# Optimization experiments

Measured on AMD Instinct MI355X. Metric: run time of the kernel, lower is better.

## Reference

```python
import jax, jax.numpy as jnp
import numpy as np

N_TOKENS = 8192
D_MODEL = 1024
N_EXPERT = 8
TOP_K = 2
D_HIDDEN = 4 * D_MODEL


def setup_inputs() -> dict:
    key = jax.random.key(0)
    ks = jax.random.split(key, 7)
    s_in = 1.0 / np.sqrt(D_MODEL)
    s_hid = 1.0 / np.sqrt(D_HIDDEN)
    return {
        "inp": jax.random.normal(ks[0], (N_TOKENS, D_MODEL), dtype=jnp.float32),
        "gate_w": jax.random.normal(ks[1], (D_MODEL, N_EXPERT), dtype=jnp.float32) * s_in,
        "gate_b": jnp.zeros((N_EXPERT,), dtype=jnp.float32),
        "w1": jax.random.normal(ks[2], (N_EXPERT, D_MODEL, D_HIDDEN), dtype=jnp.float32) * s_in,
        "b1": jnp.zeros((N_EXPERT, D_HIDDEN), dtype=jnp.float32),
        "w2": jax.random.normal(ks[3], (N_EXPERT, D_HIDDEN, D_MODEL), dtype=jnp.float32) * s_hid,
        "b2": jnp.zeros((N_EXPERT, D_MODEL), dtype=jnp.float32),
    }


def reference(inp, gate_w, gate_b, w1, b1, w2, b2):
    # NaiveGate: linear logits -> top_k -> softmax over the selected k logits
    logits = inp @ gate_w + gate_b                      # [N, E]
    top_vals, top_idx = jax.lax.top_k(logits, TOP_K)    # [N, K]
    gate_score = jax.nn.softmax(top_vals, axis=-1)      # [N, K]

    # Dispatch/combine: y[n] = sum_k score[n,k] * expert_{idx[n,k]}(x[n]).
    # Loop over the small fixed expert set; mask-weighted accumulate replaces
    # the scatter / grouped-GEMM / gather of the original (same math).
    y = jnp.zeros_like(inp)
    for e in range(N_EXPERT):
        h = jax.nn.gelu(inp @ w1[e] + b1[e])             # [N, H]
        o = h @ w2[e] + b2[e]                            # [N, D]
        w_e = jnp.sum(gate_score * (top_idx == e), axis=-1)  # [N]
        y = y + w_e[:, None] * o
    return y
```

## Files before the change

kernel.cpp:

```cpp
#include <hip/hip_runtime.h>
#include <hip/hip_bf16.h>

#define NT 8192
#define DM 1024
#define NE 8
#define DH 4096
#define NP (NT * 2)

typedef __attribute__((ext_vector_type(8))) __bf16 bf16x8;
typedef __attribute__((ext_vector_type(4))) float f32x4;

__device__ __forceinline__ ushort f2bf(float f) {
  unsigned int x = __float_as_uint(f);
  unsigned int r = (x + 0x7fffu + ((x >> 16) & 1u)) >> 16;
  return (ushort)r;
}

__device__ __forceinline__ float gelu_fast(float x) {
  float x2 = x * x;
  float t = __builtin_fmaf(x2, 0.044715f, 1.0f);
  float m = x * t * 2.3025851f;
  m = fminf(m, 126.0f);
  float p = __builtin_amdgcn_exp2f(m);
  return x * p * __builtin_amdgcn_rcpf(p + 1.0f);
}

__device__ __forceinline__ void async_copy16(const void* gsrc, void* ldst) {
  __builtin_amdgcn_global_load_lds(
      (const __attribute__((address_space(1))) void*)gsrc,
      (__attribute__((address_space(3))) void*)ldst, 16, 0, 0);
}

__global__ __launch_bounds__(256) void fused_pre_kernel(
    const float* __restrict__ w1, const float* __restrict__ w2,
    ushort* __restrict__ w1t, ushort* __restrict__ w2t,
    const float* __restrict__ inp, const float* __restrict__ gw,
    const float* __restrict__ gb, ushort* __restrict__ inp_bf,
    int* __restrict__ counts, int* __restrict__ tok_list,
    float* __restrict__ scale_list, float* __restrict__ y) {
  __shared__ ushort tileT[128][136];
  __shared__ int   lcnt[NE];
  __shared__ int   gbase[NE];
  __shared__ int   ltok[NE][64];
  __shared__ float lsc[NE][64];
  const int b = blockIdx.x;

  if (b < 128) {
    const int t = threadIdx.x;
    if (t < NE) lcnt[t] = 0;
    __syncthreads();
    const int wave = t >> 6, lane = t & 63;
    const int tokBase = b * 64 + wave * 16;
    for (int ti = 0; ti < 16; ti++) {
      const int token = tokBase + ti;
      const float* x = inp + (size_t)token * DM;
      float acc[NE];
#pragma unroll
      for (int e = 0; e < NE; e++) acc[e] = 0.f;
#pragma unroll
      for (int j = 0; j < 16; j++) {
        int idx = j * 64 + lane;
        float xv = x[idx];
        const float4* g = (const float4*)(gw + (size_t)idx * NE);
        float4 g0 = g[0], g1 = g[1];
        acc[0] += xv * g0.x; acc[1] += xv * g0.y; acc[2] += xv * g0.z; acc[3] += xv * g0.w;
        acc[4] += xv * g1.x; acc[5] += xv * g1.y; acc[6] += xv * g1.z; acc[7] += xv * g1.w;
      }
#pragma unroll
      for (int e = 0; e < NE; e++) {
        for (int off = 32; off; off >>= 1) acc[e] += __shfl_xor(acc[e], off, 64);
      }
      if (lane == 0) {
        float v[NE];
#pragma unroll
        for (int e = 0; e < NE; e++) v[e] = acc[e] + gb[e];
        int i0 = 0; float b0 = v[0];
#pragma unroll
        for (int e = 1; e < NE; e++) if (v[e] > b0) { b0 = v[e]; i0 = e; }
        int i1 = -1; float b1v = -INFINITY;
#pragma unroll
        for (int e = 0; e < NE; e++) if (e != i0 && v[e] > b1v) { b1v = v[e]; i1 = e; }
        float s1 = 1.f / (1.f + __expf(b0 - b1v));
        float s0 = 1.f - s1;
        int p0 = atomicAdd(&lcnt[i0], 1);
        ltok[i0][p0] = token; lsc[i0][p0] = s0;
        int p1 = atomicAdd(&lcnt[i1], 1);
        ltok[i1][p1] = token; lsc[i1][p1] = s1;
      }
    }
    __syncthreads();
    if (t < NE) gbase[t] = atomicAdd(&counts[t], lcnt[t]);
    __syncthreads();
#pragma unroll
    for (int e = 0; e < NE; e++) {
      int n = lcnt[e], gb0 = gbase[e];
      for (int s = t; s < n; s += 256) {
        tok_list[e * NT + gb0 + s] = ltok[e][s];
        scale_list[e * NT + gb0 + s] = lsc[e][s];
      }
    }
  } else if (b < 4224) {
    const int tb = b - 128;
    const int which = tb >> 11;
    const int rem = tb & 2047;
    const int e = rem >> 8;
    const int bb = rem & 255;
    const float* src;
    ushort* dst;
    int R, C, r0, c0;
    if (which == 0) {
      src = w1 + (size_t)e * DM * DH; dst = w1t + (size_t)e * DM * DH;
      R = DM; C = DH;
      r0 = (bb & 7) * 128;   c0 = (bb >> 3) * 128;
    } else {
      src = w2 + (size_t)e * DM * DH; dst = w2t + (size_t)e * DM * DH;
      R = DH; C = DM;
      r0 = (bb & 31) * 128;  c0 = (bb >> 5) * 128;
    }
    const int tx = threadIdx.x & 31;
    const int ty = threadIdx.x >> 5;
#pragma unroll
    for (int i = 0; i < 4; i++) {
      int rb = ty + 8 * i;
      const float* sp = src + (size_t)(r0 + 4 * rb) * C + c0 + 4 * tx;
      float4 a0 = *(const float4*)(sp);
      float4 a1 = *(const float4*)(sp + C);
      float4 a2 = *(const float4*)(sp + 2 * (size_t)C);
      float4 a3 = *(const float4*)(sp + 3 * (size_t)C);
      ushort4 o0 = { f2bf(a0.x), f2bf(a1.x), f2bf(a2.x), f2bf(a3.x) };
      ushort4 o1 = { f2bf(a0.y), f2bf(a1.y), f2bf(a2.y), f2bf(a3.y) };
      ushort4 o2 = { f2bf(a0.z), f2bf(a1.z), f2bf(a2.z), f2bf(a3.z) };
      ushort4 o3 = { f2bf(a0.w), f2bf(a1.w), f2bf(a2.w), f2bf(a3.w) };
      *(ushort4*)(&tileT[4 * tx + 0][4 * rb]) = o0;
      *(ushort4*)(&tileT[4 * tx + 1][4 * rb]) = o1;
      *(ushort4*)(&tileT[4 * tx + 2][4 * rb]) = o2;
      *(ushort4*)(&tileT[4 * tx + 3][4 * rb]) = o3;
    }
    __syncthreads();
    const int kx = threadIdx.x & 31;
    const int ny = threadIdx.x >> 5;
#pragma unroll
    for (int i = 0; i < 16; i++) {
      int n = ny + 8 * i;
      *(ushort4*)(dst + (size_t)(c0 + n) * R + r0 + 4 * kx) =
          *(const ushort4*)(&tileT[n][4 * kx]);
    }
  } else if (b < 6272) {
    const int idx = b - 4224;
    const float4* s4 = (const float4*)(inp + (size_t)idx * 4096);
    ushort4* d4 = (ushort4*)(inp_bf + (size_t)idx * 4096);
    const int t = threadIdx.x;
#pragma unroll
    for (int j = 0; j < 4; j++) {
      float4 v = s4[t + j * 256];
      ushort4 o = { f2bf(v.x), f2bf(v.y), f2bf(v.z), f2bf(v.w) };
      d4[t + j * 256] = o;
    }
  } else {
    const int idx = b - 6272;
    float4* dst = (float4*)(y + (size_t)idx * 4096);
    f32x4 z = {0.f, 0.f, 0.f, 0.f};
#pragma unroll
    for (int j = 0; j < 4; j++)
      ((f32x4*)dst)[j * 256 + threadIdx.x] = z;
  }
}


#define STAGE_TILE(base)                                      \
  do {                                                        \
    async_copy16(aP0, (char*)(base) + wv * 1024);             \
    async_copy16(aP1, (char*)(base) + 4096 + wv * 1024);      \
    async_copy16(bP0, (char*)(base) + 8192 + wv * 1024);      \
    async_copy16(bP1, (char*)(base) + 12288 + wv * 1024);     \
    aP0 += 32; aP1 += 32; bP0 += 32; bP1 += 32;               \
  } while (0)

__global__ __launch_bounds__(256) void gemm1_kernel(
    const ushort* __restrict__ xbf, const ushort* __restrict__ w1t,
    const float* __restrict__ b1, const int* __restrict__ tok_list,
    const int* __restrict__ counts, ushort* __restrict__ hbuf) {
  const int b = blockIdx.x;
  const int e = b & 7;
  const int idx = b >> 3;
  const int mTile = idx & 63;
  const int nTile = idx >> 6;
  int off = 0;
  for (int i = 0; i < e; i++) off += counts[i];
  const int cnt = counts[e];
  if (mTile * 128 >= cnt) return;

  __shared__ __attribute__((aligned(128))) char ldsB[49152];

  const int t = threadIdx.x;
  const int lane = t & 63, wv = t >> 6;
  const int wm = wv & 1, wn = wv >> 1;

  const int sr = t >> 2;
  const int sc = (((t & 3) ^ ((sr >> 1) & 3)) * 8);
  int gi0 = mTile * 128 + sr;      if (gi0 >= cnt) gi0 = cnt - 1;
  int gi1 = mTile * 128 + 64 + sr; if (gi1 >= cnt) gi1 = cnt - 1;
  const int tok0 = tok_list[e * NT + gi0];
  const int tok1 = tok_list[e * NT + gi1];
  const ushort* aP0 = xbf + (size_t)tok0 * DM + sc;
  const ushort* aP1 = xbf + (size_t)tok1 * DM + sc;
  const ushort* bP0 = w1t + ((size_t)e * DH + nTile * 128 + sr) * DM + sc;
  const ushort* bP1 = bP0 + (size_t)64 * DM;

  f32x4 zero = {0.f, 0.f, 0.f, 0.f};
  f32x4 acc[4][4];
#pragma unroll
  for (int i = 0; i < 4; i++)
#pragma unroll
    for (int j = 0; j < 4; j++) acc[i][j] = zero;

  const int quad = lane >> 4, lc = lane & 15;
  const int rq = quad ^ ((lc >> 1) & 3);

  auto compute = [&](const char* buf) {
    const char* A_ = buf;
    const char* B_ = buf + 8192;
    bf16x8 af[4], bfr[4];
#pragma unroll
    for (int mi = 0; mi < 4; mi++) {
      int row = wm * 64 + mi * 16 + lc;
      af[mi] = *(const bf16x8*)(A_ + row * 64 + rq * 16);
    }
#pragma unroll
    for (int ni = 0; ni < 4; ni++) {
      int row = wn * 64 + ni * 16 + lc;
      bfr[ni] = *(const bf16x8*)(B_ + row * 64 + rq * 16);
    }
#pragma unroll
    for (int mi = 0; mi < 4; mi++)
#pragma unroll
      for (int ni = 0; ni < 4; ni++)
        acc[mi][ni] = __builtin_amdgcn_mfma_f32_16x16x32_bf16(af[mi], bfr[ni], acc[mi][ni], 0, 0, 0);
  };

  const int NIT = DM / 32;
  STAGE_TILE(ldsB);
  STAGE_TILE(ldsB + 16384);
  int cur = 0;
  for (int tt = 0; tt < NIT - 1; ++tt) {
    asm volatile("s_waitcnt vmcnt(4)" ::: "memory");
    __builtin_amdgcn_s_barrier();
    if (tt + 2 < NIT) {
      int nx = cur + 2; if (nx >= 3) nx -= 3;
      STAGE_TILE(ldsB + nx * 16384);
    }
    compute(ldsB + cur * 16384);
    cur = (cur == 2) ? 0 : cur + 1;
  }
  asm volatile("s_waitcnt vmcnt(0)" ::: "memory");
  __builtin_amdgcn_s_barrier();
  compute(ldsB + cur * 16384);

  float bias[4];
#pragma unroll
  for (int ni = 0; ni < 4; ni++)
    bias[ni] = b1[(size_t)e * DH + nTile * 128 + wn * 64 + ni * 16 + lc];

#pragma unroll
  for (int mi = 0; mi < 4; mi++) {
#pragma unroll
    for (int r = 0; r < 4; r++) {
      int lr = wm * 64 + mi * 16 + quad * 4 + r;
      int gi = mTile * 128 + lr;
      if (gi < cnt) {
        ushort* hrow = hbuf + (size_t)(off + gi) * DH + nTile * 128 + wn * 64 + lc;
#pragma unroll
        for (int ni = 0; ni < 4; ni++) {
          float v = acc[mi][ni][r] + bias[ni];
          hrow[ni * 16] = f2bf(gelu_fast(v));
        }
      }
    }
  }
}

__global__ __launch_bounds__(256) void gemm2_kernel(
    const ushort* __restrict__ hbuf, const ushort* __restrict__ w2t,
    const float* __restrict__ b2, const int* __restrict__ tok_list,
    const float* __restrict__ scale_list, const int* __restrict__ counts,
    float* __restrict__ y) {
  const int b = blockIdx.x;
  const int e = b & 7;
  const int idx = b >> 3;
  const int nTile = idx & 7;
  const int mTile = idx >> 3;
  int off = 0;
  for (int i = 0; i < e; i++) off += counts[i];
  const int cnt = counts[e];
  if (mTile * 128 >= cnt) return;

  __shared__ __attribute__((aligned(128))) char ldsB[49152];

  const int t = threadIdx.x;
  const int lane = t & 63, wv = t >> 6;
  const int wm = wv & 1, wn = wv >> 1;

  const int sr = t >> 2;
  const int sc = (((t & 3) ^ ((sr >> 1) & 3)) * 8);
  int gi0 = mTile * 128 + sr;      if (gi0 >= cnt) gi0 = cnt - 1;
  int gi1 = mTile * 128 + 64 + sr; if (gi1 >= cnt) gi1 = cnt - 1;
  const ushort* aP0 = hbuf + (size_t)(off + gi0) * DH + sc;
  const ushort* aP1 = hbuf + (size_t)(off + gi1) * DH + sc;
  const ushort* bP0 = w2t + ((size_t)e * DM + nTile * 128 + sr) * DH + sc;
  const ushort* bP1 = bP0 + (size_t)64 * DH;

  f32x4 zero = {0.f, 0.f, 0.f, 0.f};
  f32x4 acc[4][4];
#pragma unroll
  for (int i = 0; i < 4; i++)
#pragma unroll
    for (int j = 0; j < 4; j++) acc[i][j] = zero;

  const int quad = lane >> 4, lc = lane & 15;
  const int rq = quad ^ ((lc >> 1) & 3);

  auto compute = [&](const char* buf) {
    const char* A_ = buf;
    const char* B_ = buf + 8192;
    bf16x8 af[4], bfr[4];
#pragma unroll
    for (int mi = 0; mi < 4; mi++) {
      int row = wm * 64 + mi * 16 + lc;
      af[mi] = *(const bf16x8*)(A_ + row * 64 + rq * 16);
    }
#pragma unroll
    for (int ni = 0; ni < 4; ni++) {
      int row = wn * 64 + ni * 16 + lc;
      bfr[ni] = *(const bf16x8*)(B_ + row * 64 + rq * 16);
    }
#pragma unroll
    for (int mi = 0; mi < 4; mi++)
#pragma unroll
      for (int ni = 0; ni < 4; ni++)
        acc[mi][ni] = __builtin_amdgcn_mfma_f32_16x16x32_bf16(af[mi], bfr[ni], acc[mi][ni], 0, 0, 0);
  };

  const int NIT = DH / 32;
  STAGE_TILE(ldsB);
  STAGE_TILE(ldsB + 16384);
  int cur = 0;
  for (int tt = 0; tt < NIT - 1; ++tt) {
    asm volatile("s_waitcnt vmcnt(4)" ::: "memory");
    __builtin_amdgcn_s_barrier();
    if (tt + 2 < NIT) {
      int nx = cur + 2; if (nx >= 3) nx -= 3;
      STAGE_TILE(ldsB + nx * 16384);
    }
    compute(ldsB + cur * 16384);
    cur = (cur == 2) ? 0 : cur + 1;
  }
  asm volatile("s_waitcnt vmcnt(0)" ::: "memory");
  __builtin_amdgcn_s_barrier();
  compute(ldsB + cur * 16384);

  float bias[4];
#pragma unroll
  for (int ni = 0; ni < 4; ni++)
    bias[ni] = b2[(size_t)e * DM + nTile * 128 + wn * 64 + ni * 16 + lc];

#pragma unroll
  for (int mi = 0; mi < 4; mi++) {
#pragma unroll
    for (int r = 0; r < 4; r++) {
      int lr = wm * 64 + mi * 16 + quad * 4 + r;
      int gi = mTile * 128 + lr;
      if (gi < cnt) {
        int tok = tok_list[e * NT + gi];
        float s = scale_list[e * NT + gi];
        float* yrow = y + (size_t)tok * DM + nTile * 128 + wn * 64 + lc;
#pragma unroll
        for (int ni = 0; ni < 4; ni++) {
          float v = (acc[mi][ni][r] + bias[ni]) * s;
          unsafeAtomicAdd(&yrow[ni * 16], v);
        }
      }
    }
  }
}

extern "C" void kernel_launch(void* const* d_in, const int* in_sizes, int n_in,
                              void* d_out, int out_size, void* d_ws, size_t ws_size,
                              hipStream_t stream) {
  const float* inp = (const float*)d_in[0];
  const float* gw  = (const float*)d_in[1];
  const float* gb  = (const float*)d_in[2];
  const float* w1  = (const float*)d_in[3];
  const float* b1  = (const float*)d_in[4];
  const float* w2  = (const float*)d_in[5];
  const float* b2  = (const float*)d_in[6];
  float* y = (float*)d_out;

  char* ws = (char*)d_ws;
  ushort* inp_bf = (ushort*)ws;              ws += (size_t)NT * DM * 2;
  ushort* w1t    = (ushort*)ws;              ws += (size_t)NE * DH * DM * 2;
  ushort* w2t    = (ushort*)ws;              ws += (size_t)NE * DM * DH * 2;
  ushort* hbuf   = (ushort*)ws;              ws += (size_t)NP * DH * 2;
  int*    tok_list   = (int*)ws;             ws += (size_t)NE * NT * 4;
  float*  scale_list = (float*)ws;           ws += (size_t)NE * NT * 4;
  int*    counts     = (int*)ws;             ws += 256;

  hipMemsetAsync(counts, 0, 256, stream);

  fused_pre_kernel<<<8320, 256, 0, stream>>>(w1, w2, w1t, w2t, inp, gw, gb,
                                             inp_bf, counts, tok_list, scale_list, y);
  gemm1_kernel<<<NE * 32 * 64, 256, 0, stream>>>(inp_bf, w1t, b1, tok_list, counts, hbuf);
  gemm2_kernel<<<NE * 8 * 64, 256, 0, stream>>>(hbuf, w2t, b2, tok_list, scale_list, counts, y);
}
```

Baseline: 752.8 us.

## Rewrite gemm2 with 256x256 tiles, 8 waves and a phased double-buffered pipeline

The down-projection GEMM moves from 128x128 tiles with 4 waves and a 3-stage K=32 ring buffer to 256x256 tiles with 8 waves, K=64 steps and a 128KB double-buffered LDS. Each K step is split into four quadrant phases. Each phase interleaves async global-to-LDS staging of the next tile with MFMA work and raises wave priority around the MFMA bursts. The aim is more operand reuse per byte loaded and better overlap of loads with matrix math. The cost is one block per CU, larger per-tile padding waste for uneven expert counts, and prefetch reads past the end of each row on the final iteration.

```diff
diff --git a/kernel.cpp b/kernel.cpp
--- a/kernel.cpp
+++ b/kernel.cpp
@@ -166,7 +166,6 @@
   }
 }
 
-
 #define STAGE_TILE(base)                                      \
   do {                                                        \
     async_copy16(aP0, (char*)(base) + wv * 1024);             \
@@ -279,7 +278,7 @@
   }
 }
 
-__global__ __launch_bounds__(256) void gemm2_kernel(
+__global__ __launch_bounds__(512, 2) void gemm2_kernel(
     const ushort* __restrict__ hbuf, const ushort* __restrict__ w2t,
     const float* __restrict__ b2, const int* __restrict__ tok_list,
     const float* __restrict__ scale_list, const int* __restrict__ counts,
@@ -287,96 +286,185 @@
   const int b = blockIdx.x;
   const int e = b & 7;
   const int idx = b >> 3;
-  const int nTile = idx & 7;
-  const int mTile = idx >> 3;
+  const int nTile = idx & 3;
+  const int mTile = idx >> 2;
   int off = 0;
   for (int i = 0; i < e; i++) off += counts[i];
   const int cnt = counts[e];
-  if (mTile * 128 >= cnt) return;
-
-  __shared__ __attribute__((aligned(128))) char ldsB[49152];
-
-  const int t = threadIdx.x;
-  const int lane = t & 63, wv = t >> 6;
-  const int wm = wv & 1, wn = wv >> 1;
-
-  const int sr = t >> 2;
-  const int sc = (((t & 3) ^ ((sr >> 1) & 3)) * 8);
-  int gi0 = mTile * 128 + sr;      if (gi0 >= cnt) gi0 = cnt - 1;
-  int gi1 = mTile * 128 + 64 + sr; if (gi1 >= cnt) gi1 = cnt - 1;
-  const ushort* aP0 = hbuf + (size_t)(off + gi0) * DH + sc;
-  const ushort* aP1 = hbuf + (size_t)(off + gi1) * DH + sc;
-  const ushort* bP0 = w2t + ((size_t)e * DM + nTile * 128 + sr) * DH + sc;
-  const ushort* bP1 = bP0 + (size_t)64 * DH;
+  if (mTile * 256 >= cnt) return;
+
+  __shared__ __attribute__((aligned(128))) char ldsB[131072];
+
+  const int tid = threadIdx.x;
+  const int lane = tid & 63;
+  const int wv = tid >> 6;
+  const int wm = wv >> 2;
+  const int wn = wv & 3;
+  const int quad = lane >> 4, lc = lane & 15;
+
+  const int rl0 = tid >> 3;
+  const int rl1 = rl0 + 64;
+  const int s8 = tid & 7;
+  const int k0sw0 = (s8 ^ (rl0 & 7)) * 8;
+  const int k0sw1 = (s8 ^ (rl1 & 7)) * 8;
+  int gA[4];
+#pragma unroll
+  for (int h = 0; h < 2; h++) {
+    int g0 = mTile * 256 + h * 128 + rl0; if (g0 >= cnt) g0 = cnt - 1;
+    int g1 = mTile * 256 + h * 128 + rl1; if (g1 >= cnt) g1 = cnt - 1;
+    gA[h * 2 + 0] = g0; gA[h * 2 + 1] = g1;
+  }
+  const ushort* aP00 = hbuf + (size_t)(off + gA[0]) * DH + k0sw0;
+  const ushort* aP01 = hbuf + (size_t)(off + gA[1]) * DH + k0sw1;
+  const ushort* aP10 = hbuf + (size_t)(off + gA[2]) * DH + k0sw0;
+  const ushort* aP11 = hbuf + (size_t)(off + gA[3]) * DH + k0sw1;
+  const size_t bRow = (size_t)e * DM + nTile * 256;
+  const ushort* bP00 = w2t + (bRow + rl0) * DH + k0sw0;
+  const ushort* bP01 = w2t + (bRow + rl1) * DH + k0sw1;
+  const ushort* bP10 = w2t + (bRow + 128 + rl0) * DH + k0sw0;
+  const ushort* bP11 = w2t + (bRow + 128 + rl1) * DH + k0sw1;
+
+  const int sw0 = ((0 + quad) ^ (lc & 7)) * 16;
+  const int sw1 = ((4 + quad) ^ (lc & 7)) * 16;
+  const int aRow0 = (wm * 64 + lc) * 128;
+  const int bRow0 = (wn * 32 + lc) * 128;
 
   f32x4 zero = {0.f, 0.f, 0.f, 0.f};
-  f32x4 acc[4][4];
-#pragma unroll
-  for (int i = 0; i < 4; i++)
+  f32x4 acc[8][4];
+#pragma unroll
+  for (int i = 0; i < 8; i++)
 #pragma unroll
     for (int j = 0; j < 4; j++) acc[i][j] = zero;
 
-  const int quad = lane >> 4, lc = lane & 15;
-  const int rq = quad ^ ((lc >> 1) & 3);
-
-  auto compute = [&](const char* buf) {
-    const char* A_ = buf;
-    const char* B_ = buf + 8192;
-    bf16x8 af[4], bfr[4];
+  bf16x8 af0[4][2], af1[4][2], bfr[2][2];
+
+#define STG_A0(nbB) do { async_copy16(aP00, (nbB) + tid * 16);                 \
+                         async_copy16(aP01, (nbB) + 8192 + tid * 16); } while (0)
+#define STG_A1(nbB) do { async_copy16(aP10, (nbB) + 16384 + tid * 16);         \
+                         async_copy16(aP11, (nbB) + 16384 + 8192 + tid * 16); } while (0)
+#define STG_B0(nbB) do { async_copy16(bP00, (nbB) + 32768 + tid * 16);         \
+                         async_copy16(bP01, (nbB) + 32768 + 8192 + tid * 16); } while (0)
+#define STG_B1(nbB) do { async_copy16(bP10, (nbB) + 49152 + tid * 16);         \
+                         async_copy16(bP11, (nbB) + 49152 + 8192 + tid * 16); } while (0)
+#define ADV8() do { aP00 += 64; aP01 += 64; aP10 += 64; aP11 += 64;            \
+                    bP00 += 64; bP01 += 64; bP10 += 64; bP11 += 64; } while (0)
+
+  STG_A0(ldsB); STG_B0(ldsB); STG_A1(ldsB); STG_B1(ldsB);
+  ADV8();
+  asm volatile("s_waitcnt vmcnt(4)" ::: "memory");
+  __builtin_amdgcn_s_barrier();
+
+  const int NTIT = DH / 64;
+  for (int t = 0; t < NTIT; ++t) {
+    const char* cA = ldsB + (t & 1) * 65536;
+    const char* cB = cA + 32768;
+    char* nbB = ldsB + ((t & 1) ^ 1) * 65536;
+
 #pragma unroll
     for (int mi = 0; mi < 4; mi++) {
-      int row = wm * 64 + mi * 16 + lc;
-      af[mi] = *(const bf16x8*)(A_ + row * 64 + rq * 16);
-    }
-#pragma unroll
-    for (int ni = 0; ni < 4; ni++) {
-      int row = wn * 64 + ni * 16 + lc;
-      bfr[ni] = *(const bf16x8*)(B_ + row * 64 + rq * 16);
-    }
+      af0[mi][0] = *(const bf16x8*)(cA + aRow0 + mi * 2048 + sw0);
+      af0[mi][1] = *(const bf16x8*)(cA + aRow0 + mi * 2048 + sw1);
+    }
+#pragma unroll
+    for (int j = 0; j < 2; j++) {
+      bfr[j][0] = *(const bf16x8*)(cB + bRow0 + j * 2048 + sw0);
+      bfr[j][1] = *(const bf16x8*)(cB + bRow0 + j * 2048 + sw1);
+    }
+    STG_A0(nbB);
+    asm volatile("s_waitcnt vmcnt(4)" ::: "memory");
+    __builtin_amdgcn_s_barrier();
+    asm volatile("s_waitcnt lgkmcnt(0)" ::: "memory");
+    __builtin_amdgcn_sched_barrier(0);
+    __builtin_amdgcn_s_setprio(1);
 #pragma unroll
     for (int mi = 0; mi < 4; mi++)
 #pragma unroll
-      for (int ni = 0; ni < 4; ni++)
-        acc[mi][ni] = __builtin_amdgcn_mfma_f32_16x16x32_bf16(af[mi], bfr[ni], acc[mi][ni], 0, 0, 0);
-  };
-
-  const int NIT = DH / 32;
-  STAGE_TILE(ldsB);
-  STAGE_TILE(ldsB + 16384);
-  int cur = 0;
-  for (int tt = 0; tt < NIT - 1; ++tt) {
+      for (int j = 0; j < 2; j++) {
+        acc[mi][j] = __builtin_amdgcn_mfma_f32_16x16x32_bf16(af0[mi][0], bfr[j][0], acc[mi][j], 0, 0, 0);
+        acc[mi][j] = __builtin_amdgcn_mfma_f32_16x16x32_bf16(af0[mi][1], bfr[j][1], acc[mi][j], 0, 0, 0);
+      }
+    __builtin_amdgcn_s_setprio(0);
+    __builtin_amdgcn_s_barrier();
+
+#pragma unroll
+    for (int mi = 0; mi < 4; mi++) {
+      af1[mi][0] = *(const bf16x8*)(cA + 16384 + aRow0 + mi * 2048 + sw0);
+      af1[mi][1] = *(const bf16x8*)(cA + 16384 + aRow0 + mi * 2048 + sw1);
+    }
+    STG_B0(nbB);
     asm volatile("s_waitcnt vmcnt(4)" ::: "memory");
     __builtin_amdgcn_s_barrier();
-    if (tt + 2 < NIT) {
-      int nx = cur + 2; if (nx >= 3) nx -= 3;
-      STAGE_TILE(ldsB + nx * 16384);
-    }
-    compute(ldsB + cur * 16384);
-    cur = (cur == 2) ? 0 : cur + 1;
-  }
-  asm volatile("s_waitcnt vmcnt(0)" ::: "memory");
-  __builtin_amdgcn_s_barrier();
-  compute(ldsB + cur * 16384);
+    asm volatile("s_waitcnt lgkmcnt(0)" ::: "memory");
+    __builtin_amdgcn_sched_barrier(0);
+    __builtin_amdgcn_s_setprio(1);
+#pragma unroll
+    for (int mi = 0; mi < 4; mi++)
+#pragma unroll
+      for (int j = 0; j < 2; j++) {
+        acc[4 + mi][j] = __builtin_amdgcn_mfma_f32_16x16x32_bf16(af1[mi][0], bfr[j][0], acc[4 + mi][j], 0, 0, 0);
+        acc[4 + mi][j] = __builtin_amdgcn_mfma_f32_16x16x32_bf16(af1[mi][1], bfr[j][1], acc[4 + mi][j], 0, 0, 0);
+      }
+    __builtin_amdgcn_s_setprio(0);
+    __builtin_amdgcn_s_barrier();
+
+#pragma unroll
+    for (int j = 0; j < 2; j++) {
+      bfr[j][0] = *(const bf16x8*)(cB + 16384 + bRow0 + j * 2048 + sw0);
+      bfr[j][1] = *(const bf16x8*)(cB + 16384 + bRow0 + j * 2048 + sw1);
+    }
+    STG_A1(nbB);
+    __builtin_amdgcn_s_barrier();
+    asm volatile("s_waitcnt lgkmcnt(0)" ::: "memory");
+    __builtin_amdgcn_sched_barrier(0);
+    __builtin_amdgcn_s_setprio(1);
+#pragma unroll
+    for (int mi = 0; mi < 4; mi++)
+#pragma unroll
+      for (int j = 0; j < 2; j++) {
+        acc[4 + mi][2 + j] = __builtin_amdgcn_mfma_f32_16x16x32_bf16(af1[mi][0], bfr[j][0], acc[4 + mi][2 + j], 0, 0, 0);
+        acc[4 + mi][2 + j] = __builtin_amdgcn_mfma_f32_16x16x32_bf16(af1[mi][1], bfr[j][1], acc[4 + mi][2 + j], 0, 0, 0);
+      }
+    __builtin_amdgcn_s_setprio(0);
+    __builtin_amdgcn_s_barrier();
+
+    STG_B1(nbB);
+    asm volatile("s_waitcnt vmcnt(4)" ::: "memory");
+    __builtin_amdgcn_s_barrier();
+    __builtin_amdgcn_s_setprio(1);
+#pragma unroll
+    for (int mi = 0; mi < 4; mi++)
+#pragma unroll
+      for (int j = 0; j < 2; j++) {
+        acc[mi][2 + j] = __builtin_amdgcn_mfma_f32_16x16x32_bf16(af0[mi][0], bfr[j][0], acc[mi][2 + j], 0, 0, 0);
+        acc[mi][2 + j] = __builtin_amdgcn_mfma_f32_16x16x32_bf16(af0[mi][1], bfr[j][1], acc[mi][2 + j], 0, 0, 0);
+      }
+    __builtin_amdgcn_s_setprio(0);
+    __builtin_amdgcn_s_barrier();
+
+    ADV8();
+  }
 
   float bias[4];
 #pragma unroll
-  for (int ni = 0; ni < 4; ni++)
-    bias[ni] = b2[(size_t)e * DM + nTile * 128 + wn * 64 + ni * 16 + lc];
-
-#pragma unroll
-  for (int mi = 0; mi < 4; mi++) {
+  for (int ni = 0; ni < 4; ni++) {
+    int col = (ni >> 1) * 128 + wn * 32 + (ni & 1) * 16 + lc;
+    bias[ni] = b2[(size_t)e * DM + nTile * 256 + col];
+  }
+#pragma unroll
+  for (int mi = 0; mi < 8; mi++) {
+    int rowbase = (mi >> 2) * 128 + wm * 64 + (mi & 3) * 16;
 #pragma unroll
     for (int r = 0; r < 4; r++) {
-      int lr = wm * 64 + mi * 16 + quad * 4 + r;
-      int gi = mTile * 128 + lr;
+      int gi = mTile * 256 + rowbase + quad * 4 + r;
       if (gi < cnt) {
         int tok = tok_list[e * NT + gi];
         float s = scale_list[e * NT + gi];
-        float* yrow = y + (size_t)tok * DM + nTile * 128 + wn * 64 + lc;
+        float* yrow = y + (size_t)tok * DM + nTile * 256;
 #pragma unroll
         for (int ni = 0; ni < 4; ni++) {
+          int col = (ni >> 1) * 128 + wn * 32 + (ni & 1) * 16 + lc;
           float v = (acc[mi][ni][r] + bias[ni]) * s;
-          unsafeAtomicAdd(&yrow[ni * 16], v);
+          unsafeAtomicAdd(&yrow[col], v);
         }
       }
     }
@@ -409,5 +497,5 @@
   fused_pre_kernel<<<8320, 256, 0, stream>>>(w1, w2, w1t, w2t, inp, gw, gb,
                                              inp_bf, counts, tok_list, scale_list, y);
   gemm1_kernel<<<NE * 32 * 64, 256, 0, stream>>>(inp_bf, w1t, b1, tok_list, counts, hbuf);
-  gemm2_kernel<<<NE * 8 * 64, 256, 0, stream>>>(hbuf, w2t, b2, tok_list, scale_list, counts, y);
-}
+  gemm2_kernel<<<NE * 32 * 4, 512, 0, stream>>>(hbuf, w2t, b2, tok_list, scale_list, counts, y);
+}
```

Measured after the change: 790.6 us. 5.0% more time.
